# Kernel optimization log

Measured on AMD Instinct MI355X. Metric: run time of the kernel, lower is better.

## Reference

```python
import jax, jax.numpy as jnp
import numpy as np

B, A, D, H, F = 256, 96, 384, 192, 96   # molecules, atoms, feat, hidden, species-MLP out
S = 4                                   # number of species (H, C, N, O)
E = B * A * 32                          # edges (avg degree 32)
CUTOFF = 5.2


def smooth_cutoff(d, cutoff):
    # Smoothstep-style cutoff: 1 at d=0, smoothly -> 0 at d=cutoff (Smoothstep class, reversed edges)
    x = jnp.clip((cutoff - d) / cutoff, 0.0, 1.0)
    return x ** 3 * (x * (6.0 * x - 15.0) + 10.0)


def setup_inputs() -> dict:
    key = jax.random.key(0)
    ks = jax.random.split(key, 9)
    species = jax.random.randint(ks[0], (B, A), 0, S, dtype=jnp.int32)
    in_features = jax.random.normal(ks[1], (B, A, D), dtype=jnp.float32)
    atom_index12 = jax.random.randint(ks[2], (2, E), 0, B * A, dtype=jnp.int32)
    distances = jax.random.uniform(ks[3], (E,), jnp.float32, 0.1, CUTOFF)
    total_charges = jnp.zeros((B,), jnp.float32)
    W1 = jax.random.normal(ks[4], (S, D, H), jnp.float32) / np.float32(np.sqrt(D))
    W2 = jax.random.normal(ks[5], (S, H, F), jnp.float32) / np.float32(np.sqrt(H))
    Wn = jax.random.normal(ks[6], (S, F, F), jnp.float32) / np.float32(np.sqrt(F))
    Wf = jax.random.normal(ks[7], (S, 2 * F, 1), jnp.float32) / np.float32(np.sqrt(2 * F))
    return dict(species=species, in_features=in_features, atom_index12=atom_index12,
                distances=distances, total_charges=total_charges,
                W1=W1, W2=W2, Wn=Wn, Wf=Wf,
                decay_prefactor=jnp.asarray(1.0, jnp.float32),
                decay_factor=jnp.asarray(1.0, jnp.float32))


def reference(species, in_features, atom_index12, distances, total_charges,
              W1, W2, Wn, Wf, decay_prefactor, decay_factor):
    b, a, d = in_features.shape
    n = b * a
    sp = species.reshape(-1)                      # [N]
    x = in_features.reshape(n, d)                 # [N, D]

    # per-species main MLP dispatch: internal[i] = MLP_{sp[i]}(x[i])
    internal = jnp.zeros((n, F), x.dtype)
    for s in range(S):
        mask = (sp == s)[:, None]
        h = jax.nn.gelu(x @ W1[s]) @ W2[s]        # [N, F]
        internal = internal + jnp.where(mask, h, jnp.zeros((), x.dtype))

    # per-species neighbor MLP
    nbr = jnp.zeros((n, F), x.dtype)
    for s in range(S):
        mask = (sp == s)[:, None]
        nbr = nbr + jnp.where(mask, internal @ Wn[s], jnp.zeros((), x.dtype))

    # distance-decayed edge messages: merged[i0] += nbr[i1]*w, merged[i1] += nbr[i0]*w
    decay = (decay_prefactor ** 2) * jnp.exp(-(decay_factor ** 2) * distances) \
            * smooth_cutoff(distances, CUTOFF)    # [E]
    i0, i1 = atom_index12[0], atom_index12[1]
    m_to_i0 = nbr[i1] * decay[:, None]            # [E, F]
    m_to_i1 = nbr[i0] * decay[:, None]
    merged = jax.ops.segment_sum(jnp.concatenate([m_to_i0, m_to_i1], axis=0),
                                 jnp.concatenate([i0, i1], axis=0),
                                 num_segments=n)  # [N, F]

    feats = jnp.concatenate([internal, merged], axis=-1)  # [N, 2F]

    # per-species final head -> precharges
    precharges = jnp.zeros((n,), x.dtype)
    for s in range(S):
        mask = (sp == s)
        precharges = precharges + jnp.where(mask, (feats @ Wf[s])[:, 0], jnp.zeros((), x.dtype))
    precharges = precharges.reshape(b, a)

    # total-charge redistribution (uniform factors, no learned redistribution)
    dummy_mask = species != -1
    factors = 1.0 / dummy_mask.sum(-1, keepdims=True).astype(x.dtype)
    charges = precharges + (total_charges - precharges.sum(-1))[:, None] * factors
    charges = jnp.where(dummy_mask, charges, jnp.zeros((), x.dtype))
    return species, charges, precharges
```

## Files before the change

### kernel.cpp

```cpp
#include <hip/hip_runtime.h>
#include <cstdint>
#include <cstddef>

#define NBm 256
#define NAm 96
#define NDm 384
#define NHm 192
#define NFm 96
#define NSm 4
#define NATOMS (NBm*NAm)
#define NEe (NATOMS*32)
#define NMSG (2*NEe)
#define HBLK 1536
#define CUTOFF_ 5.2f

typedef __attribute__((ext_vector_type(8))) short short8;
typedef __attribute__((ext_vector_type(4))) float float4v;
typedef __attribute__((ext_vector_type(2))) int int2v;

__device__ __forceinline__ short f2bf(float f){
  union { float f; unsigned u; } v; v.f = f;
  unsigned r = v.u + 0x7FFFu + ((v.u >> 16) & 1u);
  return (short)(r >> 16);
}

__device__ __forceinline__ float gelu_t(float x){
  float u = 0.7978845608028654f * (x + 0.044715f * x*x*x);
  float e = __expf(-2.0f * fabsf(u));
  float t = (1.0f - e) / (1.0f + e);
  t = (u >= 0.f) ? t : -t;
  return 0.5f * x * (1.0f + t);
}

#define W1N (NSm*NDm*NHm)
#define W2N (NSm*NHm*NFm)
#define WNN (NSm*NFm*NFm)
__global__ void k_wprep(const float* __restrict__ W1, const float* __restrict__ W2,
                        const float* __restrict__ Wn,
                        short* __restrict__ W1t, short* __restrict__ W2t,
                        short* __restrict__ Wnt, int* __restrict__ spc){
  if (blockIdx.x == 0 && threadIdx.x < NSm) spc[threadIdx.x] = 0;
  int idx = blockIdx.x*256 + threadIdx.x;
  if (idx < W1N){
    int s = idx / (NDm*NHm); int rem = idx - s*NDm*NHm;
    int k = rem / NHm, c = rem - k*NHm;
    W1t[(s*NHm + c)*NDm + k] = f2bf(W1[idx]);
  } else if (idx < W1N + W2N){
    int j = idx - W1N;
    int s = j / (NHm*NFm); int rem = j - s*NHm*NFm;
    int k = rem / NFm, c = rem - k*NFm;
    W2t[(s*NFm + c)*NHm + k] = f2bf(W2[j]);
  } else if (idx < W1N + W2N + WNN){
    int j = idx - W1N - W2N;
    int s = j / (NFm*NFm); int rem = j - s*NFm*NFm;
    int k = rem / NFm, c = rem - k*NFm;
    Wnt[(s*NFm + c)*NFm + k] = f2bf(Wn[j]);
  }
}

__global__ void k_spcount(const int* __restrict__ sp, int* __restrict__ spc){
  __shared__ int h[NSm];
  int t = threadIdx.x;
  if (t < NSm) h[t] = 0;
  __syncthreads();
  int i = blockIdx.x*256 + t;
  atomicAdd(&h[sp[i]], 1);
  __syncthreads();
  if (t < NSm) atomicAdd(&spc[t], h[t]);
}

__global__ void k_spscan(const int* __restrict__ spc, int* __restrict__ sps, int* __restrict__ spcur){
  if (threadIdx.x==0 && blockIdx.x==0){
    int r=0;
    for (int s=0;s<NSm;s++){ sps[s]=r; spcur[s]=r; r+=spc[s]; }
    sps[NSm]=r;
  }
}

__global__ void k_spscatter(const int* __restrict__ sp, int* __restrict__ spcur,
                            int* __restrict__ order){
  __shared__ int h[NSm], base[NSm];
  int t = threadIdx.x;
  if (t < NSm) h[t]=0;
  __syncthreads();
  int i = blockIdx.x*256 + t;
  int s = sp[i];
  int lr = atomicAdd(&h[s], 1);
  __syncthreads();
  if (t < NSm) base[t] = atomicAdd(&spcur[t], h[t]);
  __syncthreads();
  order[base[s] + lr] = i;
}

__global__ __launch_bounds__(256) void k_mlp(
    const float* __restrict__ X, const int* __restrict__ order,
    const int* __restrict__ sps,
    const short* __restrict__ W1t, const short* __restrict__ W2t,
    const short* __restrict__ Wnt, const float* __restrict__ Wf,
    float* __restrict__ pre, float* __restrict__ nbr_g){
  const int s = blockIdx.y;
  const int s0 = sps[s];
  const int cnt = sps[s+1] - s0;
  const int row0 = blockIdx.x * 64;
  if (row0 >= cnt) return;

  __shared__ short Hs[64][200];
  __shared__ short Ws[192*40];
  __shared__ short Is[64][104];
  __shared__ int aids[64];

  const int tid = threadIdx.x;
  if (tid < 64){
    int r = row0 + tid;
    aids[tid] = order[s0 + ((r < cnt) ? r : 0)];
  }
  __syncthreads();

  const int wave = tid >> 6, lane = tid & 63;
  const int lrow = lane & 15, quad = lane >> 4;
  const int arow = wave*16 + lrow;
  const float* xrow = X + (size_t)aids[arow]*NDm + quad*8;

  short8 afs[12];
  #pragma unroll
  for (int kb=0; kb<12; kb++){
    const float* p = xrow + kb*32;
    #pragma unroll
    for (int j=0;j<8;j++) afs[kb][j] = f2bf(p[j]);
  }

  const short* W1s = W1t + (size_t)s*NHm*NDm;
  float4v acc[12];
  #pragma unroll
  for (int i=0;i<12;i++){ acc[i][0]=0.f; acc[i][1]=0.f; acc[i][2]=0.f; acc[i][3]=0.f; }

  for (int kb=0; kb<12; kb++){
    __syncthreads();
    for (int e = tid; e < 192*4; e += 256){
      int c = e >> 2, kq = (e & 3) * 8;
      *(short8*)(&Ws[c*40 + kq]) = *(const short8*)(W1s + c*NDm + kb*32 + kq);
    }
    __syncthreads();
    short8 af = afs[kb];
    #pragma unroll
    for (int ct=0; ct<12; ct++){
      short8 bfb = *(const short8*)(&Ws[(ct*16 + lrow)*40 + quad*8]);
      acc[ct] = __builtin_amdgcn_mfma_f32_16x16x32_bf16(af, bfb, acc[ct], 0,0,0);
    }
  }
  #pragma unroll
  for (int ct=0; ct<12; ct++){
    #pragma unroll
    for (int r=0;r<4;r++){
      Hs[wave*16 + quad*4 + r][ct*16 + lrow] = f2bf(gelu_t(acc[ct][r]));
    }
  }

  const short* W2s = W2t + (size_t)s*NFm*NHm;
  float4v acc2[6];
  #pragma unroll
  for (int i=0;i<6;i++){ acc2[i][0]=0.f; acc2[i][1]=0.f; acc2[i][2]=0.f; acc2[i][3]=0.f; }
  for (int kb=0; kb<6; kb++){
    __syncthreads();
    for (int e = tid; e < 96*4; e += 256){
      int c = e >> 2, kq = (e & 3) * 8;
      *(short8*)(&Ws[c*40 + kq]) = *(const short8*)(W2s + c*NHm + kb*32 + kq);
    }
    __syncthreads();
    short8 af2 = *(const short8*)(&Hs[wave*16 + lrow][kb*32 + quad*8]);
    #pragma unroll
    for (int ct=0; ct<6; ct++){
      short8 bfb = *(const short8*)(&Ws[(ct*16 + lrow)*40 + quad*8]);
      acc2[ct] = __builtin_amdgcn_mfma_f32_16x16x32_bf16(af2, bfb, acc2[ct], 0,0,0);
    }
  }
  #pragma unroll
  for (int ct=0; ct<6; ct++){
    #pragma unroll
    for (int r=0;r<4;r++){
      Is[wave*16 + quad*4 + r][ct*16 + lrow] = f2bf(acc2[ct][r]);
    }
  }

  {
    float pr[4] = {0.f,0.f,0.f,0.f};
    #pragma unroll
    for (int ct=0; ct<6; ct++){
      float wv = Wf[s*2*NFm + ct*16 + lrow];
      #pragma unroll
      for (int r=0;r<4;r++) pr[r] += acc2[ct][r] * wv;
    }
    #pragma unroll
    for (int m=1; m<16; m<<=1){
      #pragma unroll
      for (int r=0;r<4;r++) pr[r] += __shfl_xor(pr[r], m, 64);
    }
    if (lrow == 0){
      #pragma unroll
      for (int r=0;r<4;r++){
        int row = wave*16 + quad*4 + r;
        if (row0 + row < cnt) pre[aids[row]] = pr[r];
      }
    }
  }

  const short* Wns = Wnt + (size_t)s*NFm*NFm;
  float4v acc3[6];
  #pragma unroll
  for (int i=0;i<6;i++){ acc3[i][0]=0.f; acc3[i][1]=0.f; acc3[i][2]=0.f; acc3[i][3]=0.f; }
  for (int kb=0; kb<3; kb++){
    __syncthreads();
    for (int e = tid; e < 96*4; e += 256){
      int c = e >> 2, kq = (e & 3) * 8;
      *(short8*)(&Ws[c*40 + kq]) = *(const short8*)(Wns + c*NFm + kb*32 + kq);
    }
    __syncthreads();
    short8 af3 = *(const short8*)(&Is[wave*16 + lrow][kb*32 + quad*8]);
    #pragma unroll
    for (int ct=0; ct<6; ct++){
      short8 bfb = *(const short8*)(&Ws[(ct*16 + lrow)*40 + quad*8]);
      acc3[ct] = __builtin_amdgcn_mfma_f32_16x16x32_bf16(af3, bfb, acc3[ct], 0,0,0);
    }
  }
  #pragma unroll
  for (int ct=0; ct<6; ct++){
    #pragma unroll
    for (int r=0;r<4;r++){
      int row = wave*16 + quad*4 + r, col = ct*16 + lrow;
      if (row0 + row < cnt) nbr_g[(size_t)aids[row]*NFm + col] = acc3[ct][r];
    }
  }
}

__global__ void k_nd4(const float* __restrict__ nbr, const float* __restrict__ Wf,
                      float* __restrict__ nd4){
  int a = blockIdx.x*4 + (threadIdx.x >> 6);
  int lane = threadIdx.x & 63;
  bool lo = lane < 32;
  const float* np = nbr + (size_t)a*NFm;
  float nv1 = np[lane];
  float nv2 = lo ? np[64+lane] : 0.f;
  const float* w0 = Wf + 0*2*NFm + NFm;
  const float* w1 = Wf + 1*2*NFm + NFm;
  const float* w2 = Wf + 2*2*NFm + NFm;
  const float* w3 = Wf + 3*2*NFm + NFm;
  float n0 = nv1*w0[lane] + (lo ? nv2*w0[64+lane] : 0.f);
  float n1 = nv1*w1[lane] + (lo ? nv2*w1[64+lane] : 0.f);
  float n2 = nv1*w2[lane] + (lo ? nv2*w2[64+lane] : 0.f);
  float n3 = nv1*w3[lane] + (lo ? nv2*w3[64+lane] : 0.f);
  #pragma unroll
  for (int m=1; m<64; m<<=1){
    n0 += __shfl_xor(n0, m, 64);
    n1 += __shfl_xor(n1, m, 64);
    n2 += __shfl_xor(n2, m, 64);
    n3 += __shfl_xor(n3, m, 64);
  }
  if (lane == 0){
    float4v v; v[0]=n0; v[1]=n1; v[2]=n2; v[3]=n3;
    *(float4v*)(nd4 + (size_t)a*4) = v;
  }
}

__global__ __launch_bounds__(1024) void k_hist(const int* __restrict__ ai,
                                               int* __restrict__ Hist){
  __shared__ int h[NBm];
  int t = threadIdx.x;
  if (t < NBm) h[t] = 0;
  __syncthreads();
  int m = blockIdx.x*1024 + t;
  int mol = ai[m] / NAm;
  atomicAdd(&h[mol], 1);
  __syncthreads();
  if (t < NBm) Hist[blockIdx.x*NBm + t] = h[t];
}

__global__ void k_mscan(int* __restrict__ Hist, int* __restrict__ Tot){
  __shared__ int sums[256];
  int mol = blockIdx.x, t = threadIdx.x;
  int v[6]; int loc = 0;
  #pragma unroll
  for (int j=0;j<6;j++){ v[j] = Hist[(t*6+j)*NBm + mol]; loc += v[j]; }
  sums[t] = loc; __syncthreads();
  for (int off=1; off<256; off<<=1){
    int x = (t >= off) ? sums[t-off] : 0;
    __syncthreads();
    sums[t] += x;
    __syncthreads();
  }
  int run = sums[t] - loc;
  #pragma unroll
  for (int j=0;j<6;j++){ Hist[(t*6+j)*NBm + mol] = run; run += v[j]; }
  if (t == 255) Tot[mol] = run;
}

__global__ void k_segscan(const int* __restrict__ Tot, int* __restrict__ Seg){
  __shared__ int s[256];
  int t = threadIdx.x;
  int v = Tot[t]; s[t] = v; __syncthreads();
  for (int off=1; off<256; off<<=1){
    int x = (t >= off) ? s[t-off] : 0;
    __syncthreads();
    s[t] += x;
    __syncthreads();
  }
  Seg[t] = s[t] - v;
  if (t == 255) Seg[256] = s[255];
}

__global__ __launch_bounds__(1024) void k_scatter(const int* __restrict__ ai,
    const float* __restrict__ dist, const float* __restrict__ pref,
    const float* __restrict__ fac, const int* __restrict__ Hist,
    const int* __restrict__ Seg, int2v* __restrict__ Msg){
  __shared__ int cnt[NBm];
  __shared__ int off[NBm];
  int t = threadIdx.x;
  if (t < NBm){ cnt[t] = 0; off[t] = Seg[t] + Hist[blockIdx.x*NBm + t]; }
  __syncthreads();
  int m = blockIdx.x*1024 + t;
  int dest = ai[m];
  int other = ai[(m < NEe) ? m + NEe : m - NEe];
  int e = (m < NEe) ? m : m - NEe;
  float d = dist[e];
  float x = (CUTOFF_ - d) * (1.0f/CUTOFF_);
  x = fminf(fmaxf(x, 0.f), 1.f);
  float sc = x*x*x*(x*(6.f*x - 15.f) + 10.f);
  float p = pref[0], fc = fac[0];
  float w = p*p * expf(-fc*fc*d) * sc;
  int mol = dest / NAm, dl = dest - mol*NAm;
  int rank = atomicAdd(&cnt[mol], 1);
  int2v msg; msg[0] = (other << 7) | dl; msg[1] = __float_as_int(w);
  Msg[off[mol] + rank] = msg;
}

__global__ __launch_bounds__(256) void k_accum(const int* __restrict__ Seg,
    const int2v* __restrict__ Msg, const float* __restrict__ nd4,
    const int* __restrict__ sp, const float* __restrict__ pre,
    const float* __restrict__ tc, float* __restrict__ out){
  __shared__ float acc[NAm];
  __shared__ int spl[NAm];
  __shared__ float red[128];
  int mol = blockIdx.x, t = threadIdx.x;
  if (t < NAm){ acc[t] = 0.f; spl[t] = sp[mol*NAm + t]; }
  __syncthreads();
  int s0 = Seg[mol], s1 = Seg[mol+1];
  for (int i = s0 + t; i < s1; i += 256){
    int2v kw = Msg[i];
    int key = kw[0]; float w = __int_as_float(kw[1]);
    int dl = key & 127, other = key >> 7;
    float val = w * nd4[(size_t)other*4 + spl[dl]];
    atomicAdd(&acc[dl], val);
  }
  __syncthreads();
  float pch = 0.f;
  if (t < NAm) pch = pre[mol*NAm + t] + acc[t];
  if (t < 128) red[t] = (t < NAm) ? pch : 0.f;
  __syncthreads();
  for (int o=64; o>0; o>>=1){
    if (t < o) red[t] += red[t + o];
    __syncthreads();
  }
  float sum = red[0];
  if (t < NAm){
    float c = pch + (tc[mol] - sum) * (1.0f/96.0f);
    out[mol*NAm + t] = (float)spl[t];
    out[NATOMS + mol*NAm + t] = c;
    out[2*NATOMS + mol*NAm + t] = pch;
  }
}

extern "C" void kernel_launch(void* const* d_in, const int* in_sizes, int n_in,
                              void* d_out, int out_size, void* d_ws, size_t ws_size,
                              hipStream_t stream) {
  const int*   species = (const int*)  d_in[0];
  const float* X       = (const float*)d_in[1];
  const int*   ai      = (const int*)  d_in[2];
  const float* dist    = (const float*)d_in[3];
  const float* tc      = (const float*)d_in[4];
  const float* W1      = (const float*)d_in[5];
  const float* W2      = (const float*)d_in[6];
  const float* Wn      = (const float*)d_in[7];
  const float* Wf      = (const float*)d_in[8];
  const float* pref    = (const float*)d_in[9];
  const float* fac     = (const float*)d_in[10];
  float* out = (float*)d_out;

  char* w = (char*)d_ws;
  auto alloc = [&](size_t bytes)->char*{
    char* p = w; w += (bytes + 255) & ~(size_t)255; return p;
  };
  int*   spc   = (int*)  alloc(64);
  int*   sps   = (int*)  alloc(64);
  int*   spcur = (int*)  alloc(64);
  int*   order = (int*)  alloc((size_t)NATOMS*4);
  float* nd4   = (float*)alloc((size_t)NATOMS*4*4);
  float* pre   = (float*)alloc((size_t)NATOMS*4);
  float* nbr   = (float*)alloc((size_t)NATOMS*NFm*4);
  short* W1t   = (short*)alloc((size_t)W1N*2);
  short* W2t   = (short*)alloc((size_t)W2N*2);
  short* Wnt   = (short*)alloc((size_t)WNN*2);
  int*   Hist  = (int*)  alloc((size_t)HBLK*NBm*4);
  int*   Tot   = (int*)  alloc(1024);
  int*   Seg   = (int*)  alloc((NBm+1)*4);
  int2v* Msg   = (int2v*)alloc((size_t)NMSG*8);

  k_wprep<<<(W1N+W2N+WNN)/256, 256, 0, stream>>>(W1, W2, Wn, W1t, W2t, Wnt, spc);
  k_spcount<<<NATOMS/256, 256, 0, stream>>>(species, spc);
  k_spscan<<<1, 64, 0, stream>>>(spc, sps, spcur);
  k_spscatter<<<NATOMS/256, 256, 0, stream>>>(species, spcur, order);
  dim3 g(NATOMS/64, NSm);
  k_mlp<<<g, 256, 0, stream>>>(X, order, sps, W1t, W2t, Wnt, Wf, pre, nbr);
  k_nd4<<<NATOMS/4, 256, 0, stream>>>(nbr, Wf, nd4);
  k_hist<<<HBLK, 1024, 0, stream>>>(ai, Hist);
  k_mscan<<<NBm, 256, 0, stream>>>(Hist, Tot);
  k_segscan<<<1, 256, 0, stream>>>(Tot, Seg);
  k_scatter<<<HBLK, 1024, 0, stream>>>(ai, dist, pref, fac, Hist, Seg, Msg);
  k_accum<<<NBm, 256, 0, stream>>>(Seg, Msg, nd4, species, pre, tc, out);
}
```

Before: 190.9 us.

## Double-buffer weight tiles in MLP kernel and merge species count/scan kernels

The MLP kernel now keeps two shared-memory weight buffers and prefetches the next k-slice from global memory into registers while the MFMAs on the current slice run, which removes one barrier per iteration and hides load latency. Separately, the species histogram and prefix scan are merged into a single one-block kernel, dropping one launch and the global atomics. This costs extra shared memory, which may lower occupancy, and the single block serialises a count over 24K atoms.

```diff
diff --git a/kernel.cpp b/kernel.cpp
--- a/kernel.cpp
+++ b/kernel.cpp
@@ -38,8 +38,7 @@
 __global__ void k_wprep(const float* __restrict__ W1, const float* __restrict__ W2,
                         const float* __restrict__ Wn,
                         short* __restrict__ W1t, short* __restrict__ W2t,
-                        short* __restrict__ Wnt, int* __restrict__ spc){
-  if (blockIdx.x == 0 && threadIdx.x < NSm) spc[threadIdx.x] = 0;
+                        short* __restrict__ Wnt){
   int idx = blockIdx.x*256 + threadIdx.x;
   if (idx < W1N){
     int s = idx / (NDm*NHm); int rem = idx - s*NDm*NHm;
@@ -58,22 +57,18 @@
   }
 }
 
-__global__ void k_spcount(const int* __restrict__ sp, int* __restrict__ spc){
+__global__ void k_spinit(const int* __restrict__ sp, int* __restrict__ sps,
+                         int* __restrict__ spcur){
   __shared__ int h[NSm];
   int t = threadIdx.x;
   if (t < NSm) h[t] = 0;
   __syncthreads();
-  int i = blockIdx.x*256 + t;
-  atomicAdd(&h[sp[i]], 1);
-  __syncthreads();
-  if (t < NSm) atomicAdd(&spc[t], h[t]);
-}
-
-__global__ void k_spscan(const int* __restrict__ spc, int* __restrict__ sps, int* __restrict__ spcur){
-  if (threadIdx.x==0 && blockIdx.x==0){
-    int r=0;
-    for (int s=0;s<NSm;s++){ sps[s]=r; spcur[s]=r; r+=spc[s]; }
-    sps[NSm]=r;
+  for (int i = t; i < NATOMS; i += 1024) atomicAdd(&h[sp[i]], 1);
+  __syncthreads();
+  if (t == 0){
+    int r = 0;
+    for (int s=0;s<NSm;s++){ sps[s]=r; spcur[s]=r; r += h[s]; }
+    sps[NSm] = r;
   }
 }
 
@@ -105,7 +100,7 @@
   if (row0 >= cnt) return;
 
   __shared__ short Hs[64][200];
-  __shared__ short Ws[192*40];
+  __shared__ short Ws[2][192*40];
   __shared__ short Is[64][104];
   __shared__ int aids[64];
 
@@ -129,23 +124,45 @@
     for (int j=0;j<8;j++) afs[kb][j] = f2bf(p[j]);
   }
 
+  const int e0 = tid,        c0 = e0 >> 2, q0 = (e0 & 3) * 8;
+  const int e1 = tid + 256,  c1 = e1 >> 2, q1 = (e1 & 3) * 8;
+  const int e2 = tid + 512,  c2 = e2 >> 2, q2 = (e2 & 3) * 8;
+  const bool h2 = tid < 128;
+
   const short* W1s = W1t + (size_t)s*NHm*NDm;
   float4v acc[12];
   #pragma unroll
   for (int i=0;i<12;i++){ acc[i][0]=0.f; acc[i][1]=0.f; acc[i][2]=0.f; acc[i][3]=0.f; }
-
+  {
+    short8 r0 = *(const short8*)(W1s + c0*NDm + q0);
+    short8 r1 = *(const short8*)(W1s + c1*NDm + q1);
+    short8 r2 = *(const short8*)(W1s + c2*NDm + q2);
+    *(short8*)(&Ws[0][c0*40 + q0]) = r0;
+    *(short8*)(&Ws[0][c1*40 + q1]) = r1;
+    *(short8*)(&Ws[0][c2*40 + q2]) = r2;
+  }
+  __syncthreads();
   for (int kb=0; kb<12; kb++){
-    __syncthreads();
-    for (int e = tid; e < 192*4; e += 256){
-      int c = e >> 2, kq = (e & 3) * 8;
-      *(short8*)(&Ws[c*40 + kq]) = *(const short8*)(W1s + c*NDm + kb*32 + kq);
-    }
-    __syncthreads();
+    short8 r0, r1, r2;
+    if (kb < 11){
+      const short* src = W1s + (kb+1)*32;
+      r0 = *(const short8*)(src + c0*NDm + q0);
+      r1 = *(const short8*)(src + c1*NDm + q1);
+      r2 = *(const short8*)(src + c2*NDm + q2);
+    }
+    const short* wb = Ws[kb & 1];
     short8 af = afs[kb];
     #pragma unroll
     for (int ct=0; ct<12; ct++){
-      short8 bfb = *(const short8*)(&Ws[(ct*16 + lrow)*40 + quad*8]);
+      short8 bfb = *(const short8*)(wb + (ct*16 + lrow)*40 + quad*8);
       acc[ct] = __builtin_amdgcn_mfma_f32_16x16x32_bf16(af, bfb, acc[ct], 0,0,0);
+    }
+    if (kb < 11){
+      short* wn = Ws[(kb+1) & 1];
+      *(short8*)(wn + c0*40 + q0) = r0;
+      *(short8*)(wn + c1*40 + q1) = r1;
+      *(short8*)(wn + c2*40 + q2) = r2;
+      __syncthreads();
     }
   }
   #pragma unroll
@@ -160,18 +177,33 @@
   float4v acc2[6];
   #pragma unroll
   for (int i=0;i<6;i++){ acc2[i][0]=0.f; acc2[i][1]=0.f; acc2[i][2]=0.f; acc2[i][3]=0.f; }
+  {
+    short8 r0 = *(const short8*)(W2s + c0*NHm + q0);
+    short8 r1;
+    if (h2) r1 = *(const short8*)(W2s + c1*NHm + q1);
+    *(short8*)(&Ws[0][c0*40 + q0]) = r0;
+    if (h2) *(short8*)(&Ws[0][c1*40 + q1]) = r1;
+  }
+  __syncthreads();
   for (int kb=0; kb<6; kb++){
-    __syncthreads();
-    for (int e = tid; e < 96*4; e += 256){
-      int c = e >> 2, kq = (e & 3) * 8;
-      *(short8*)(&Ws[c*40 + kq]) = *(const short8*)(W2s + c*NHm + kb*32 + kq);
-    }
-    __syncthreads();
+    short8 r0, r1;
+    if (kb < 5){
+      const short* src = W2s + (kb+1)*32;
+      r0 = *(const short8*)(src + c0*NHm + q0);
+      if (h2) r1 = *(const short8*)(src + c1*NHm + q1);
+    }
+    const short* wb = Ws[kb & 1];
     short8 af2 = *(const short8*)(&Hs[wave*16 + lrow][kb*32 + quad*8]);
     #pragma unroll
     for (int ct=0; ct<6; ct++){
-      short8 bfb = *(const short8*)(&Ws[(ct*16 + lrow)*40 + quad*8]);
+      short8 bfb = *(const short8*)(wb + (ct*16 + lrow)*40 + quad*8);
       acc2[ct] = __builtin_amdgcn_mfma_f32_16x16x32_bf16(af2, bfb, acc2[ct], 0,0,0);
+    }
+    if (kb < 5){
+      short* wn = Ws[(kb+1) & 1];
+      *(short8*)(wn + c0*40 + q0) = r0;
+      if (h2) *(short8*)(wn + c1*40 + q1) = r1;
+      __syncthreads();
     }
   }
   #pragma unroll
@@ -208,18 +240,33 @@
   float4v acc3[6];
   #pragma unroll
   for (int i=0;i<6;i++){ acc3[i][0]=0.f; acc3[i][1]=0.f; acc3[i][2]=0.f; acc3[i][3]=0.f; }
+  {
+    short8 r0 = *(const short8*)(Wns + c0*NFm + q0);
+    short8 r1;
+    if (h2) r1 = *(const short8*)(Wns + c1*NFm + q1);
+    *(short8*)(&Ws[0][c0*40 + q0]) = r0;
+    if (h2) *(short8*)(&Ws[0][c1*40 + q1]) = r1;
+  }
+  __syncthreads();
   for (int kb=0; kb<3; kb++){
-    __syncthreads();
-    for (int e = tid; e < 96*4; e += 256){
-      int c = e >> 2, kq = (e & 3) * 8;
-      *(short8*)(&Ws[c*40 + kq]) = *(const short8*)(Wns + c*NFm + kb*32 + kq);
-    }
-    __syncthreads();
+    short8 r0, r1;
+    if (kb < 2){
+      const short* src = Wns + (kb+1)*32;
+      r0 = *(const short8*)(src + c0*NFm + q0);
+      if (h2) r1 = *(const short8*)(src + c1*NFm + q1);
+    }
+    const short* wb = Ws[kb & 1];
     short8 af3 = *(const short8*)(&Is[wave*16 + lrow][kb*32 + quad*8]);
     #pragma unroll
     for (int ct=0; ct<6; ct++){
-      short8 bfb = *(const short8*)(&Ws[(ct*16 + lrow)*40 + quad*8]);
+      short8 bfb = *(const short8*)(wb + (ct*16 + lrow)*40 + quad*8);
       acc3[ct] = __builtin_amdgcn_mfma_f32_16x16x32_bf16(af3, bfb, acc3[ct], 0,0,0);
+    }
+    if (kb < 2){
+      short* wn = Ws[(kb+1) & 1];
+      *(short8*)(wn + c0*40 + q0) = r0;
+      if (h2) *(short8*)(wn + c1*40 + q1) = r1;
+      __syncthreads();
     }
   }
   #pragma unroll
@@ -388,7 +435,6 @@
   auto alloc = [&](size_t bytes)->char*{
     char* p = w; w += (bytes + 255) & ~(size_t)255; return p;
   };
-  int*   spc   = (int*)  alloc(64);
   int*   sps   = (int*)  alloc(64);
   int*   spcur = (int*)  alloc(64);
   int*   order = (int*)  alloc((size_t)NATOMS*4);
@@ -403,9 +449,8 @@
   int*   Seg   = (int*)  alloc((NBm+1)*4);
   int2v* Msg   = (int2v*)alloc((size_t)NMSG*8);
 
-  k_wprep<<<(W1N+W2N+WNN)/256, 256, 0, stream>>>(W1, W2, Wn, W1t, W2t, Wnt, spc);
-  k_spcount<<<NATOMS/256, 256, 0, stream>>>(species, spc);
-  k_spscan<<<1, 64, 0, stream>>>(spc, sps, spcur);
+  k_wprep<<<(W1N+W2N+WNN)/256, 256, 0, stream>>>(W1, W2, Wn, W1t, W2t, Wnt);
+  k_spinit<<<1, 1024, 0, stream>>>(species, sps, spcur);
   k_spscatter<<<NATOMS/256, 256, 0, stream>>>(species, spcur, order);
   dim3 g(NATOMS/64, NSm);
   k_mlp<<<g, 256, 0, stream>>>(X, order, sps, W1t, W2t, Wnt, Wf, pre, nbr);
```

New measurement: 191.0 us. About the same (+0.1%).

## Halve MLP row tile with 2x2 wave split; merge species count and scan

Applied to the files above, without the earlier changes.

The per-species MLP kernel now handles 32 rows per block instead of 64. Its four waves are arranged as a 2x2 grid over rows and output columns, and the precharge partial sums are combined through shared memory. This doubles the block count, raises occupancy and shrinks per-thread accumulators, but every block now reloads the same weight tiles, so weight traffic per row doubles. Separately, the species count and scan kernels are merged into one single-block kernel, removing a launch and the global atomics.

```diff
diff --git a/kernel.cpp b/kernel.cpp
--- a/kernel.cpp
+++ b/kernel.cpp
@@ -38,8 +38,7 @@
 __global__ void k_wprep(const float* __restrict__ W1, const float* __restrict__ W2,
                         const float* __restrict__ Wn,
                         short* __restrict__ W1t, short* __restrict__ W2t,
-                        short* __restrict__ Wnt, int* __restrict__ spc){
-  if (blockIdx.x == 0 && threadIdx.x < NSm) spc[threadIdx.x] = 0;
+                        short* __restrict__ Wnt){
   int idx = blockIdx.x*256 + threadIdx.x;
   if (idx < W1N){
     int s = idx / (NDm*NHm); int rem = idx - s*NDm*NHm;
@@ -58,22 +57,18 @@
   }
 }
 
-__global__ void k_spcount(const int* __restrict__ sp, int* __restrict__ spc){
+__global__ void k_spinit(const int* __restrict__ sp, int* __restrict__ sps,
+                         int* __restrict__ spcur){
   __shared__ int h[NSm];
   int t = threadIdx.x;
   if (t < NSm) h[t] = 0;
   __syncthreads();
-  int i = blockIdx.x*256 + t;
-  atomicAdd(&h[sp[i]], 1);
-  __syncthreads();
-  if (t < NSm) atomicAdd(&spc[t], h[t]);
-}
-
-__global__ void k_spscan(const int* __restrict__ spc, int* __restrict__ sps, int* __restrict__ spcur){
-  if (threadIdx.x==0 && blockIdx.x==0){
-    int r=0;
-    for (int s=0;s<NSm;s++){ sps[s]=r; spcur[s]=r; r+=spc[s]; }
-    sps[NSm]=r;
+  for (int i = t; i < NATOMS; i += 1024) atomicAdd(&h[sp[i]], 1);
+  __syncthreads();
+  if (t == 0){
+    int r = 0;
+    for (int s=0;s<NSm;s++){ sps[s]=r; spcur[s]=r; r += h[s]; }
+    sps[NSm] = r;
   }
 }
 
@@ -101,16 +96,17 @@
   const int s = blockIdx.y;
   const int s0 = sps[s];
   const int cnt = sps[s+1] - s0;
-  const int row0 = blockIdx.x * 64;
+  const int row0 = blockIdx.x * 32;
   if (row0 >= cnt) return;
 
-  __shared__ short Hs[64][200];
+  __shared__ short Hs[32][200];
   __shared__ short Ws[192*40];
-  __shared__ short Is[64][104];
-  __shared__ int aids[64];
+  __shared__ short Is[32][104];
+  __shared__ int aids[32];
+  __shared__ float preP[32][2];
 
   const int tid = threadIdx.x;
-  if (tid < 64){
+  if (tid < 32){
     int r = row0 + tid;
     aids[tid] = order[s0 + ((r < cnt) ? r : 0)];
   }
@@ -118,7 +114,8 @@
 
   const int wave = tid >> 6, lane = tid & 63;
   const int lrow = lane & 15, quad = lane >> 4;
-  const int arow = wave*16 + lrow;
+  const int rg = wave & 1, cg = wave >> 1;
+  const int arow = rg*16 + lrow;
   const float* xrow = X + (size_t)aids[arow]*NDm + quad*8;
 
   short8 afs[12];
@@ -130,10 +127,9 @@
   }
 
   const short* W1s = W1t + (size_t)s*NHm*NDm;
-  float4v acc[12];
-  #pragma unroll
-  for (int i=0;i<12;i++){ acc[i][0]=0.f; acc[i][1]=0.f; acc[i][2]=0.f; acc[i][3]=0.f; }
-
+  float4v acc[6];
+  #pragma unroll
+  for (int i=0;i<6;i++){ acc[i][0]=0.f; acc[i][1]=0.f; acc[i][2]=0.f; acc[i][3]=0.f; }
   for (int kb=0; kb<12; kb++){
     __syncthreads();
     for (int e = tid; e < 192*4; e += 256){
@@ -143,23 +139,23 @@
     __syncthreads();
     short8 af = afs[kb];
     #pragma unroll
-    for (int ct=0; ct<12; ct++){
-      short8 bfb = *(const short8*)(&Ws[(ct*16 + lrow)*40 + quad*8]);
+    for (int ct=0; ct<6; ct++){
+      short8 bfb = *(const short8*)(&Ws[(cg*96 + ct*16 + lrow)*40 + quad*8]);
       acc[ct] = __builtin_amdgcn_mfma_f32_16x16x32_bf16(af, bfb, acc[ct], 0,0,0);
     }
   }
   #pragma unroll
-  for (int ct=0; ct<12; ct++){
+  for (int ct=0; ct<6; ct++){
     #pragma unroll
     for (int r=0;r<4;r++){
-      Hs[wave*16 + quad*4 + r][ct*16 + lrow] = f2bf(gelu_t(acc[ct][r]));
+      Hs[rg*16 + quad*4 + r][cg*96 + ct*16 + lrow] = f2bf(gelu_t(acc[ct][r]));
     }
   }
 
   const short* W2s = W2t + (size_t)s*NFm*NHm;
-  float4v acc2[6];
-  #pragma unroll
-  for (int i=0;i<6;i++){ acc2[i][0]=0.f; acc2[i][1]=0.f; acc2[i][2]=0.f; acc2[i][3]=0.f; }
+  float4v acc2[3];
+  #pragma unroll
+  for (int i=0;i<3;i++){ acc2[i][0]=0.f; acc2[i][1]=0.f; acc2[i][2]=0.f; acc2[i][3]=0.f; }
   for (int kb=0; kb<6; kb++){
     __syncthreads();
     for (int e = tid; e < 96*4; e += 256){
@@ -167,26 +163,26 @@
       *(short8*)(&Ws[c*40 + kq]) = *(const short8*)(W2s + c*NHm + kb*32 + kq);
     }
     __syncthreads();
-    short8 af2 = *(const short8*)(&Hs[wave*16 + lrow][kb*32 + quad*8]);
-    #pragma unroll
-    for (int ct=0; ct<6; ct++){
-      short8 bfb = *(const short8*)(&Ws[(ct*16 + lrow)*40 + quad*8]);
+    short8 af2 = *(const short8*)(&Hs[rg*16 + lrow][kb*32 + quad*8]);
+    #pragma unroll
+    for (int ct=0; ct<3; ct++){
+      short8 bfb = *(const short8*)(&Ws[(cg*48 + ct*16 + lrow)*40 + quad*8]);
       acc2[ct] = __builtin_amdgcn_mfma_f32_16x16x32_bf16(af2, bfb, acc2[ct], 0,0,0);
     }
   }
   #pragma unroll
-  for (int ct=0; ct<6; ct++){
+  for (int ct=0; ct<3; ct++){
     #pragma unroll
     for (int r=0;r<4;r++){
-      Is[wave*16 + quad*4 + r][ct*16 + lrow] = f2bf(acc2[ct][r]);
+      Is[rg*16 + quad*4 + r][cg*48 + ct*16 + lrow] = f2bf(acc2[ct][r]);
     }
   }
 
   {
     float pr[4] = {0.f,0.f,0.f,0.f};
     #pragma unroll
-    for (int ct=0; ct<6; ct++){
-      float wv = Wf[s*2*NFm + ct*16 + lrow];
+    for (int ct=0; ct<3; ct++){
+      float wv = Wf[s*2*NFm + cg*48 + ct*16 + lrow];
       #pragma unroll
       for (int r=0;r<4;r++) pr[r] += acc2[ct][r] * wv;
     }
@@ -197,17 +193,18 @@
     }
     if (lrow == 0){
       #pragma unroll
-      for (int r=0;r<4;r++){
-        int row = wave*16 + quad*4 + r;
-        if (row0 + row < cnt) pre[aids[row]] = pr[r];
-      }
-    }
+      for (int r=0;r<4;r++) preP[rg*16 + quad*4 + r][cg] = pr[r];
+    }
+  }
+  __syncthreads();
+  if (tid < 32){
+    if (row0 + tid < cnt) pre[aids[tid]] = preP[tid][0] + preP[tid][1];
   }
 
   const short* Wns = Wnt + (size_t)s*NFm*NFm;
-  float4v acc3[6];
-  #pragma unroll
-  for (int i=0;i<6;i++){ acc3[i][0]=0.f; acc3[i][1]=0.f; acc3[i][2]=0.f; acc3[i][3]=0.f; }
+  float4v acc3[3];
+  #pragma unroll
+  for (int i=0;i<3;i++){ acc3[i][0]=0.f; acc3[i][1]=0.f; acc3[i][2]=0.f; acc3[i][3]=0.f; }
   for (int kb=0; kb<3; kb++){
     __syncthreads();
     for (int e = tid; e < 96*4; e += 256){
@@ -215,18 +212,18 @@
       *(short8*)(&Ws[c*40 + kq]) = *(const short8*)(Wns + c*NFm + kb*32 + kq);
     }
     __syncthreads();
-    short8 af3 = *(const short8*)(&Is[wave*16 + lrow][kb*32 + quad*8]);
-    #pragma unroll
-    for (int ct=0; ct<6; ct++){
-      short8 bfb = *(const short8*)(&Ws[(ct*16 + lrow)*40 + quad*8]);
+    short8 af3 = *(const short8*)(&Is[rg*16 + lrow][kb*32 + quad*8]);
+    #pragma unroll
+    for (int ct=0; ct<3; ct++){
+      short8 bfb = *(const short8*)(&Ws[(cg*48 + ct*16 + lrow)*40 + quad*8]);
       acc3[ct] = __builtin_amdgcn_mfma_f32_16x16x32_bf16(af3, bfb, acc3[ct], 0,0,0);
     }
   }
   #pragma unroll
-  for (int ct=0; ct<6; ct++){
+  for (int ct=0; ct<3; ct++){
     #pragma unroll
     for (int r=0;r<4;r++){
-      int row = wave*16 + quad*4 + r, col = ct*16 + lrow;
+      int row = rg*16 + quad*4 + r, col = cg*48 + ct*16 + lrow;
       if (row0 + row < cnt) nbr_g[(size_t)aids[row]*NFm + col] = acc3[ct][r];
     }
   }
@@ -388,7 +385,6 @@
   auto alloc = [&](size_t bytes)->char*{
     char* p = w; w += (bytes + 255) & ~(size_t)255; return p;
   };
-  int*   spc   = (int*)  alloc(64);
   int*   sps   = (int*)  alloc(64);
   int*   spcur = (int*)  alloc(64);
   int*   order = (int*)  alloc((size_t)NATOMS*4);
@@ -403,11 +399,10 @@
   int*   Seg   = (int*)  alloc((NBm+1)*4);
   int2v* Msg   = (int2v*)alloc((size_t)NMSG*8);
 
-  k_wprep<<<(W1N+W2N+WNN)/256, 256, 0, stream>>>(W1, W2, Wn, W1t, W2t, Wnt, spc);
-  k_spcount<<<NATOMS/256, 256, 0, stream>>>(species, spc);
-  k_spscan<<<1, 64, 0, stream>>>(spc, sps, spcur);
+  k_wprep<<<(W1N+W2N+WNN)/256, 256, 0, stream>>>(W1, W2, Wn, W1t, W2t, Wnt);
+  k_spinit<<<1, 1024, 0, stream>>>(species, sps, spcur);
   k_spscatter<<<NATOMS/256, 256, 0, stream>>>(species, spcur, order);
-  dim3 g(NATOMS/64, NSm);
+  dim3 g(NATOMS/32, NSm);
   k_mlp<<<g, 256, 0, stream>>>(X, order, sps, W1t, W2t, Wnt, Wf, pre, nbr);
   k_nd4<<<NATOMS/4, 256, 0, stream>>>(nbr, Wf, nd4);
   k_hist<<<HBLK, 1024, 0, stream>>>(ai, Hist);
```

After: 209.1 us. +9.6%, slower.
